# Optimization experiments

Measured on AMD Instinct MI355X. Metric: run time of the kernel, lower is better.

Reference implementation:

```python
import jax, jax.numpy as jnp
import numpy as np
import math

B, S, H, NH, NKV, HD = 1, 2048, 4096, 32, 8, 128
ROPE_THETA = 10000.0


def setup_inputs() -> dict:
    key = jax.random.key(0)
    ks = jax.random.split(key, 16)
    hidden_states = jax.random.normal(ks[0], (B, S, H), jnp.float32) * 0.02
    Wq = jax.random.normal(ks[1], (NH * HD, H), jnp.float32) * 0.02
    Wk = jax.random.normal(ks[2], (NKV * HD, H), jnp.float32) * 0.02
    Wv = jax.random.normal(ks[3], (NKV * HD, H), jnp.float32) * 0.02
    Wo = jax.random.normal(ks[4], (H, NH * HD), jnp.float32) * 0.02
    # RoPE cos/sin, HF Llama convention: emb = concat(freqs, freqs)
    inv_freq = 1.0 / (ROPE_THETA ** (jnp.arange(0, HD, 2, dtype=jnp.float32) / HD))
    pos = jnp.arange(S, dtype=jnp.float32)
    freqs = pos[:, None] * inv_freq[None, :]              # [S, HD/2]
    emb = jnp.concatenate([freqs, freqs], axis=-1)        # [S, HD]
    cos = jnp.cos(emb)[None]                              # [1, S, HD]
    sin = jnp.sin(emb)[None]
    # additive causal mask [B, 1, S, S]
    causal = jnp.tril(jnp.ones((S, S), dtype=bool))
    attention_mask = jnp.where(causal, 0.0, -1e9).astype(jnp.float32)[None, None]
    # reorder permutations (as written by GPTQ act-order reordering)
    perm = lambda k, n: jax.random.permutation(k, n).astype(jnp.int32)
    return {
        'hidden_states': hidden_states, 'Wq': Wq, 'Wk': Wk, 'Wv': Wv, 'Wo': Wo,
        'cos': cos, 'sin': sin, 'attention_mask': attention_mask,
        'q_order_col': perm(ks[5], H), 'q_order_row': perm(ks[6], NH * HD),
        'k_order_col': perm(ks[7], H), 'k_order_row': perm(ks[8], NKV * HD),
        'v_order_col': perm(ks[9], H), 'v_order_row': perm(ks[10], NKV * HD),
        'o_order_col': perm(ks[11], NH * HD), 'o_order_row': perm(ks[12], H),
    }


def _rotate_half(x):
    x1, x2 = jnp.split(x, 2, axis=-1)
    return jnp.concatenate([-x2, x1], axis=-1)


def reference(hidden_states, Wq, Wk, Wv, Wo, cos, sin, attention_mask,
              q_order_col, q_order_row, k_order_col, k_order_row,
              v_order_col, v_order_row, o_order_col, o_order_row):
    bsz, q_len, _ = hidden_states.shape
    # permuted projections: gather cols of input, GEMM, gather rows of output
    q = hidden_states[:, :, q_order_col] @ Wq.T
    q = q[:, :, q_order_row]
    k = hidden_states[:, :, k_order_col] @ Wk.T
    k = k[:, :, k_order_row]
    v = hidden_states[:, :, v_order_col] @ Wv.T
    v = v[:, :, v_order_row]
    q = q.reshape(bsz, q_len, NH, HD).transpose(0, 2, 1, 3)   # [B,NH,S,HD]
    k = k.reshape(bsz, q_len, NKV, HD).transpose(0, 2, 1, 3)  # [B,NKV,S,HD]
    v = v.reshape(bsz, q_len, NKV, HD).transpose(0, 2, 1, 3)
    # RoPE
    c = cos[:, None, :, :]  # [1,1,S,HD]
    s = sin[:, None, :, :]
    q = q * c + _rotate_half(q) * s
    k = k * c + _rotate_half(k) * s
    # repeat_kv for GQA
    rep = NH // NKV
    k = jnp.repeat(k, rep, axis=1)  # [B,NH,S,HD]
    v = jnp.repeat(v, rep, axis=1)
    # eager attention: full score matrix, fp32 softmax
    scores = jnp.einsum('bhqd,bhkd->bhqk', q, k) / math.sqrt(HD)
    scores = scores + attention_mask
    probs = jax.nn.softmax(scores.astype(jnp.float32), axis=-1).astype(q.dtype)
    # dropout p=0.0 (eval) -> identity
    attn = jnp.einsum('bhqk,bhkd->bhqd', probs, v)
    attn = attn.transpose(0, 2, 1, 3).reshape(bsz, q_len, NH * HD)
    out = attn[:, :, o_order_col] @ Wo.T
    out = out[:, :, o_order_row]
    return out
```

## Files before the change

kernel.cpp:

```cpp
#include <hip/hip_runtime.h>

typedef unsigned short u16;
typedef unsigned char u8;
typedef __bf16 bf16x8 __attribute__((ext_vector_type(8)));
typedef float f32x4 __attribute__((ext_vector_type(4)));
typedef int i32x4 __attribute__((ext_vector_type(4)));
typedef int i32x8 __attribute__((ext_vector_type(8)));

__device__ __forceinline__ u16 f2bf(float f) {
    unsigned u = __float_as_uint(f);
    unsigned r = (u + 0x7fffu + ((u >> 16) & 1u)) >> 16;
    return (u16)r;
}
__device__ __forceinline__ float bf2f(u16 h) {
    return __uint_as_float(((unsigned)h) << 16);
}
__device__ __forceinline__ unsigned pack_bf2(float lo, float hi) {
    unsigned a = __float_as_uint(hi) + 0x8000u;
    unsigned b = __float_as_uint(lo) + 0x8000u;
    return __builtin_amdgcn_perm(a, b, 0x07060302u);
}
__device__ __forceinline__ unsigned pack_fp8x4(float a, float b, float c, float d) {
    unsigned w = __builtin_amdgcn_cvt_pk_fp8_f32(a, b, 0, false);
    w = __builtin_amdgcn_cvt_pk_fp8_f32(c, d, w, true);
    return w;
}
__device__ __forceinline__ void async_copy16(const void* g, void* l) {
    __builtin_amdgcn_global_load_lds((__attribute__((address_space(1))) void*)(void*)g,
                                     (__attribute__((address_space(3))) void*)l, 16, 0, 0);
}

#define FP8_SCALE 64.0f
#define FP8_UNSCALE (1.0f / 4096.0f)


__global__ void inv4_k(const int* __restrict__ q, const int* __restrict__ k,
                       const int* __restrict__ v, const int* __restrict__ o,
                       int* __restrict__ invq, int* __restrict__ invk,
                       int* __restrict__ invv, int* __restrict__ invo) {
    int i = blockIdx.x * 256 + threadIdx.x;
    int a = i >> 12, j = i & 4095;
    const int* p = a == 0 ? q : a == 1 ? k : a == 2 ? v : o;
    int* inv = a == 0 ? invq : a == 1 ? invk : a == 2 ? invv : invo;
    inv[p[j]] = j;
}

__global__ __launch_bounds__(256) void permw4_k(
    const float* __restrict__ Wq, const float* __restrict__ Wk,
    const float* __restrict__ Wv, const float* __restrict__ Wo,
    const int* __restrict__ qor, const int* __restrict__ kor,
    const int* __restrict__ vor, const int* __restrict__ oor,
    const int* __restrict__ invq, const int* __restrict__ invk,
    const int* __restrict__ invv, const int* __restrict__ invo,
    u8* __restrict__ Wqkf8, u16* __restrict__ Wvp, u16* __restrict__ Wop) {
    __shared__ float rowbuf[4096];
    int j = blockIdx.x;
    const float* W; const int* rp; const int* inv; int row; int f8;
    u8* out8 = nullptr; u16* out16 = nullptr;
    if (j < 4096)      { W = Wq; rp = qor; inv = invq; row = j;        out8 = Wqkf8 + (size_t)j * 4096; f8 = 1; }
    else if (j < 5120) { W = Wk; rp = kor; inv = invk; row = j - 4096; out8 = Wqkf8 + (size_t)j * 4096; f8 = 1; }
    else if (j < 6144) { W = Wv; rp = vor; inv = invv; row = j - 5120; out16 = Wvp + (size_t)(j - 5120) * 4096; f8 = 0; }
    else               { W = Wo; rp = oor; inv = invo; row = j - 6144; out16 = Wop + (size_t)(j - 6144) * 4096; f8 = 0; }
    if (f8) {
        int hd = row & 127, b = hd >> 4;
        row = (row & ~127) | ((hd & 15) | ((b & 1) << 6) | ((b & 2) << 3) | ((hd & 64) >> 1));
    }
    const float4* wr4 = (const float4*)(W + (size_t)rp[row] * 4096);
#pragma unroll
    for (int t = 0; t < 4; t++)
        ((float4*)rowbuf)[threadIdx.x + t * 256] = wr4[threadIdx.x + t * 256];
    __syncthreads();
    if (f8) {
        int t = threadIdx.x;
        const int4* inv4p = (const int4*)inv;
        float v[16];
#pragma unroll
        for (int u = 0; u < 4; u++) {
            int4 ix = inv4p[t * 4 + u];
            v[4 * u + 0] = rowbuf[ix.x] * FP8_SCALE;
            v[4 * u + 1] = rowbuf[ix.y] * FP8_SCALE;
            v[4 * u + 2] = rowbuf[ix.z] * FP8_SCALE;
            v[4 * u + 3] = rowbuf[ix.w] * FP8_SCALE;
        }
        uint4 wv;
        wv.x = pack_fp8x4(v[0], v[1], v[2], v[3]);
        wv.y = pack_fp8x4(v[4], v[5], v[6], v[7]);
        wv.z = pack_fp8x4(v[8], v[9], v[10], v[11]);
        wv.w = pack_fp8x4(v[12], v[13], v[14], v[15]);
        int tb = (t & ~7) | ((t & 7) ^ (j & 7));
        ((uint4*)out8)[tb] = wv;
    } else {
        unsigned* o32 = (unsigned*)out16;
        const int2* inv2 = (const int2*)inv;
#pragma unroll
        for (int t = 0; t < 8; t++) {
            int c = threadIdx.x + t * 256;
            int2 ij = inv2[c];
            o32[c] = pack_bf2(rowbuf[ij.x], rowbuf[ij.y]);
        }
    }
}

__global__ __launch_bounds__(256) void cvt_k(const float* __restrict__ x,
                                             u16* __restrict__ Xb,
                                             u8* __restrict__ Xf8) {
    int row = blockIdx.x;
    int t = threadIdx.x;
    const float4* src = (const float4*)(x + (size_t)row * 4096);
    float v[16];
#pragma unroll
    for (int u = 0; u < 4; u++) {
        float4 a = src[t * 4 + u];
        v[4 * u + 0] = a.x; v[4 * u + 1] = a.y; v[4 * u + 2] = a.z; v[4 * u + 3] = a.w;
    }
    uint4 b0, b1;
    b0.x = pack_bf2(v[0], v[1]);  b0.y = pack_bf2(v[2], v[3]);
    b0.z = pack_bf2(v[4], v[5]);  b0.w = pack_bf2(v[6], v[7]);
    b1.x = pack_bf2(v[8], v[9]);  b1.y = pack_bf2(v[10], v[11]);
    b1.z = pack_bf2(v[12], v[13]); b1.w = pack_bf2(v[14], v[15]);
    uint4* ob = (uint4*)(Xb + (size_t)row * 4096);
    ob[t * 2] = b0;
    ob[t * 2 + 1] = b1;
    uint4 w8;
    w8.x = pack_fp8x4(v[0] * FP8_SCALE, v[1] * FP8_SCALE, v[2] * FP8_SCALE, v[3] * FP8_SCALE);
    w8.y = pack_fp8x4(v[4] * FP8_SCALE, v[5] * FP8_SCALE, v[6] * FP8_SCALE, v[7] * FP8_SCALE);
    w8.z = pack_fp8x4(v[8] * FP8_SCALE, v[9] * FP8_SCALE, v[10] * FP8_SCALE, v[11] * FP8_SCALE);
    w8.w = pack_fp8x4(v[12] * FP8_SCALE, v[13] * FP8_SCALE, v[14] * FP8_SCALE, v[15] * FP8_SCALE);
    int tb = (t & ~7) | ((t & 7) ^ (row & 7));
    ((uint4*)(Xf8 + (size_t)row * 4096))[tb] = w8;
}

__global__ __launch_bounds__(256) void vtr_k(const float* __restrict__ Vpart,
                                             u16* __restrict__ Vt) {
    __shared__ u16 t[64][65];
    int bx = blockIdx.x;
    int s0 = (bx & 31) * 64, c0 = (bx >> 5) * 64;
    int x = threadIdx.x & 63, y4 = threadIdx.x >> 6;
    const float* Vp0 = Vpart;
    const float* Vp1 = Vpart + (size_t)2048 * 1024;
    for (int i = 0; i < 16; i++) {
        int r = y4 * 16 + i;
        size_t idx = (size_t)(s0 + r) * 1024 + c0 + x;
        t[r][x] = f2bf(Vp0[idx] + Vp1[idx]);
    }
    __syncthreads();
    for (int i = 0; i < 16; i++) {
        int r = y4 * 16 + i;
        int xk = 4 * (x & 15) + (x >> 4);
        Vt[(size_t)(c0 + r) * 2048 + s0 + xk] = t[x][r];
    }
}


#define QKV_BAR() asm volatile("s_barrier" ::: "memory")

#define QK_STAGE(bufi, kt) do {                                                   \
    u8* la_ = S8 + (bufi) * 32768 + w * 4096;                                     \
    u8* lb_ = la_ + 16384;                                                        \
    const int k0_ = (kt) * 128;                                                   \
    _Pragma("unroll")                                                             \
    for (int t_ = 0; t_ < 4; t_++)                                                \
        async_copy16(AgQ + (size_t)t_ * 8 * 4096 + k0_, la_ + t_ * 1024);         \
    _Pragma("unroll")                                                             \
    for (int t_ = 0; t_ < 4; t_++)                                                \
        async_copy16(BgQ + (size_t)t_ * 8 * 4096 + k0_, lb_ + t_ * 1024);         \
} while (0)

#define QK_COMPUTE(bufi) do {                                                     \
    const u8* la_ = S8 + (bufi) * 32768;                                          \
    const u8* lb_ = la_ + 16384;                                                  \
    union { i32x8 v8; i32x4 v4[2]; } u_;                                          \
    i32x8 bfv[4], af0, af1;                                                       \
    _Pragma("unroll")                                                             \
    for (int j_ = 0; j_ < 4; j_++) {                                              \
        const int r_ = (wn + j_ * 16 + l16) * 128;                                \
        u_.v4[0] = *(const i32x4*)&lb_[r_ + s0b];                                 \
        u_.v4[1] = *(const i32x4*)&lb_[r_ + s1b];                                 \
        bfv[j_] = u_.v8;                                                          \
    }                                                                             \
    { const int r_ = (wm + l16) * 128;                                            \
      u_.v4[0] = *(const i32x4*)&la_[r_ + s0b];                                   \
      u_.v4[1] = *(const i32x4*)&la_[r_ + s1b]; af0 = u_.v8; }                    \
    { const int r_ = (wm + 16 + l16) * 128;                                       \
      u_.v4[0] = *(const i32x4*)&la_[r_ + s0b];                                   \
      u_.v4[1] = *(const i32x4*)&la_[r_ + s1b]; af1 = u_.v8; }                    \
    asm volatile("s_waitcnt lgkmcnt(0)" ::: "memory");                            \
    __builtin_amdgcn_sched_barrier(0);                                            \
    __builtin_amdgcn_s_setprio(1);                                                \
    _Pragma("unroll")                                                             \
    for (int j_ = 0; j_ < 4; j_++) {                                              \
        acc[0][j_] = __builtin_amdgcn_mfma_scale_f32_16x16x128_f8f6f4(af0, bfv[j_], acc[0][j_], 0, 0, 0, 0x7F7F7F7F, 0, 0x7F7F7F7F); \
        acc[1][j_] = __builtin_amdgcn_mfma_scale_f32_16x16x128_f8f6f4(af1, bfv[j_], acc[1][j_], 0, 0, 0, 0x7F7F7F7F, 0, 0x7F7F7F7F); \
    }                                                                             \
    __builtin_amdgcn_s_setprio(0);                                                \
    { const int r_ = (wm + 32 + l16) * 128;                                       \
      u_.v4[0] = *(const i32x4*)&la_[r_ + s0b];                                   \
      u_.v4[1] = *(const i32x4*)&la_[r_ + s1b]; af0 = u_.v8; }                    \
    { const int r_ = (wm + 48 + l16) * 128;                                       \
      u_.v4[0] = *(const i32x4*)&la_[r_ + s0b];                                   \
      u_.v4[1] = *(const i32x4*)&la_[r_ + s1b]; af1 = u_.v8; }                    \
    asm volatile("s_waitcnt lgkmcnt(0)" ::: "memory");                            \
    __builtin_amdgcn_sched_barrier(0);                                            \
    __builtin_amdgcn_s_setprio(1);                                                \
    _Pragma("unroll")                                                             \
    for (int j_ = 0; j_ < 4; j_++) {                                              \
        acc[2][j_] = __builtin_amdgcn_mfma_scale_f32_16x16x128_f8f6f4(af0, bfv[j_], acc[2][j_], 0, 0, 0, 0x7F7F7F7F, 0, 0x7F7F7F7F); \
        acc[3][j_] = __builtin_amdgcn_mfma_scale_f32_16x16x128_f8f6f4(af1, bfv[j_], acc[3][j_], 0, 0, 0, 0x7F7F7F7F, 0, 0x7F7F7F7F); \
    }                                                                             \
    __builtin_amdgcn_s_setprio(0);                                                \
} while (0)

#define V_STAGE(bufi, kt) do {                                                    \
    u16* a0_ = (u16*)(S8 + (bufi) * 32768);                                       \
    u16* a1_ = a0_ + 4096;                                                        \
    u16* b0_ = a0_ + 8192;                                                        \
    u16* b1_ = a0_ + 12288;                                                       \
    const int k0_ = (kt) * 64;                                                    \
    async_copy16(AgV + k0_,                          a0_ + w * 512);              \
    async_copy16(AgV + (size_t)64 * 4096 + k0_,      a0_ + (w + 4) * 512);        \
    async_copy16(AgV + k0_ + 32,                     a1_ + w * 512);              \
    async_copy16(AgV + (size_t)64 * 4096 + k0_ + 32, a1_ + (w + 4) * 512);        \
    async_copy16(BgV + k0_,                          b0_ + w * 512);              \
    async_copy16(BgV + (size_t)64 * 4096 + k0_,      b0_ + (w + 4) * 512);        \
    async_copy16(BgV + k0_ + 32,                     b1_ + w * 512);              \
    async_copy16(BgV + (size_t)64 * 4096 + k0_ + 32, b1_ + (w + 4) * 512);        \
} while (0)

#define V_COMPUTE(bufi) do {                                                      \
    const u16* base_ = (const u16*)(S8 + (bufi) * 32768);                         \
    _Pragma("unroll")                                                             \
    for (int kk_ = 0; kk_ < 2; kk_++) {                                           \
        const u16* la_ = base_ + kk_ * 4096;                                      \
        const u16* lb_ = base_ + 8192 + kk_ * 4096;                               \
        bf16x8 af[4], bfv[4];                                                     \
        _Pragma("unroll")                                                         \
        for (int i_ = 0; i_ < 4; i_++)                                            \
            af[i_] = *(const bf16x8*)&la_[(wm + i_ * 16 + l16) * 32 + quad * 8];  \
        _Pragma("unroll")                                                         \
        for (int j_ = 0; j_ < 4; j_++)                                            \
            bfv[j_] = *(const bf16x8*)&lb_[(wn + j_ * 16 + l16) * 32 + quad * 8]; \
        asm volatile("s_waitcnt lgkmcnt(0)" ::: "memory");                        \
        __builtin_amdgcn_sched_barrier(0);                                        \
        __builtin_amdgcn_s_setprio(1);                                            \
        _Pragma("unroll")                                                         \
        for (int i_ = 0; i_ < 4; i_++)                                            \
            _Pragma("unroll")                                                     \
            for (int j_ = 0; j_ < 4; j_++)                                        \
                acc[i_][j_] = __builtin_amdgcn_mfma_f32_16x16x32_bf16(af[i_], bfv[j_], acc[i_][j_], 0, 0, 0); \
        __builtin_amdgcn_s_setprio(0);                                            \
    }                                                                             \
} while (0)

__global__ __launch_bounds__(256, 2) void gemm_qkv_k(const u8* __restrict__ Xf8,
                                                     const u16* __restrict__ Xb,
                                                     const u8* __restrict__ Wqk,
                                                     const u16* __restrict__ Wv,
                                                     u16* __restrict__ QKV,
                                                     float* __restrict__ Vpart,
                                                     const float* __restrict__ cosv,
                                                     const float* __restrict__ sinv) {
    extern __shared__ u8 S8[];
    const int tid = threadIdx.x;
    const int w = tid >> 6, lane = tid & 63;
    const int quad = lane >> 4, l16 = lane & 15;
    const int bm0 = blockIdx.y * 128;
    const int wm = (w >> 1) * 64, wn = (w & 1) * 64;
    const int swz = l16 & 7;
    const int s0b = ((quad * 2) ^ swz) * 16;
    const int s1b = ((quad * 2 + 1) ^ swz) * 16;

    if (blockIdx.x < 40) {
        const int bn0 = blockIdx.x * 128;
        const u8* AgQ = Xf8 + (size_t)(bm0 + w * 32 + (lane >> 3)) * 4096 + (lane & 7) * 16;
        const u8* BgQ = Wqk + (size_t)(bn0 + w * 32 + (lane >> 3)) * 4096 + (lane & 7) * 16;
        f32x4 acc[4][4] = {};

        QK_STAGE(0, 0);
        QK_STAGE(1, 1);
        asm volatile("s_waitcnt vmcnt(8)" ::: "memory");
        QKV_BAR();
        int cur = 0;
        for (int t = 0; t < 30; ++t) {
            QK_COMPUTE(cur);
            QKV_BAR();
            QK_STAGE(cur, t + 2);
            asm volatile("s_waitcnt vmcnt(8)" ::: "memory");
            QKV_BAR();
            cur ^= 1;
        }
        QK_COMPUTE(0);
        asm volatile("s_waitcnt vmcnt(0)" ::: "memory");
        QKV_BAR();
        QK_COMPUTE(1);

        const float qsc = (bn0 < 4096) ? 0.1275174f : 1.0f;
        const int hb = (wn ? 32 : 0) + l16;
#pragma unroll
        for (int i = 0; i < 4; i++) {
            const int row = bm0 + wm + i * 16 + quad * 4;
#pragma unroll
            for (int jp = 0; jp < 2; jp++) {
                const int d1 = hb + jp * 16;
                const int ce = bn0 + wn + jp * 32 + l16;
#pragma unroll
                for (int r = 0; r < 4; r++) {
                    const int s = row + r;
                    const float c  = cosv[s * 128 + d1];
                    const float sn = sinv[s * 128 + d1];
                    const float x1 = acc[i][jp * 2][r]     * FP8_UNSCALE;
                    const float x2 = acc[i][jp * 2 + 1][r] * FP8_UNSCALE;
                    QKV[(size_t)s * 6144 + ce]      = f2bf((x1 * c - x2 * sn) * qsc);
                    QKV[(size_t)s * 6144 + ce + 16] = f2bf((x2 * c + x1 * sn) * qsc);
                }
            }
        }
    } else {
        const int vx = blockIdx.x - 40;
        const int bn0 = (vx & 7) * 128;
        const int kslice = vx >> 3;
        const int kb = kslice * 2048;
        const int r0 = w * 16 + (lane >> 2);
        const int c0 = (lane & 3) * 8;
        const u16* AgV = Xb + (size_t)(bm0 + r0) * 4096 + kb + c0;
        const u16* BgV = Wv + (size_t)(bn0 + r0) * 4096 + kb + c0;
        f32x4 acc[4][4] = {};

        V_STAGE(0, 0);
        V_STAGE(1, 1);
        asm volatile("s_waitcnt vmcnt(8)" ::: "memory");
        QKV_BAR();
        int cur = 0;
        for (int t = 0; t < 30; ++t) {
            V_COMPUTE(cur);
            QKV_BAR();
            V_STAGE(cur, t + 2);
            asm volatile("s_waitcnt vmcnt(8)" ::: "memory");
            QKV_BAR();
            cur ^= 1;
        }
        V_COMPUTE(0);
        asm volatile("s_waitcnt vmcnt(0)" ::: "memory");
        QKV_BAR();
        V_COMPUTE(1);

        float* Vp = Vpart + (size_t)kslice * 2048 * 1024;
#pragma unroll
        for (int i = 0; i < 4; i++) {
            const int row = bm0 + wm + i * 16 + quad * 4;
#pragma unroll
            for (int j = 0; j < 4; j++) {
                const int col = bn0 + wn + j * 16 + l16;
#pragma unroll
                for (int r = 0; r < 4; r++)
                    Vp[(size_t)(row + r) * 1024 + col] = acc[i][j][r];
            }
        }
    }
}


#define GO_STAGE(bufi, kt) do {                                                   \
    u16* la_ = S + (bufi) * 24576;                                                \
    u16* lb_ = la_ + 16384;                                                       \
    const int k0_ = (kt) * 64;                                                    \
    _Pragma("unroll")                                                             \
    for (int u = 0; u < 4; u++)                                                   \
        async_copy16(Asrc + (size_t)u * 64 * 4096 + k0_, la_ + u * 4096 + sdst);  \
    _Pragma("unroll")                                                             \
    for (int u = 0; u < 2; u++)                                                   \
        async_copy16(Bsrc + (size_t)u * 64 * 4096 + k0_, lb_ + u * 4096 + sdst);  \
} while (0)

#define GO_COMPUTE(bufi) do {                                                     \
    const u16* la_ = S + (bufi) * 24576;                                          \
    const u16* lb_ = la_ + 16384;                                                 \
    bf16x8 bfr[4][2], afr[2][2];                                                  \
    _Pragma("unroll")                                                             \
    for (int j = 0; j < 4; j++) {                                                 \
        const int rb_ = (wn + j * 16 + l16) * 64;                                 \
        bfr[j][0] = *(const bf16x8*)&lb_[rb_ + o0];                               \
        bfr[j][1] = *(const bf16x8*)&lb_[rb_ + o1];                               \
    }                                                                             \
    _Pragma("unroll")                                                             \
    for (int i = 0; i < 2; i++) {                                                 \
        const int ra_ = (wm + i * 16 + l16) * 64;                                 \
        afr[i][0] = *(const bf16x8*)&la_[ra_ + o0];                               \
        afr[i][1] = *(const bf16x8*)&la_[ra_ + o1];                               \
    }                                                                             \
    asm volatile("s_waitcnt lgkmcnt(0)" ::: "memory");                            \
    __builtin_amdgcn_sched_barrier(0);                                            \
    __builtin_amdgcn_s_setprio(1);                                                \
    _Pragma("unroll")                                                             \
    for (int i = 0; i < 2; i++)                                                   \
        _Pragma("unroll")                                                         \
        for (int j = 0; j < 4; j++) {                                             \
            acc[i][j] = __builtin_amdgcn_mfma_f32_16x16x32_bf16(afr[i][0], bfr[j][0], acc[i][j], 0, 0, 0); \
            acc[i][j] = __builtin_amdgcn_mfma_f32_16x16x32_bf16(afr[i][1], bfr[j][1], acc[i][j], 0, 0, 0); \
        }                                                                         \
    __builtin_amdgcn_s_setprio(0);                                                \
    _Pragma("unroll")                                                             \
    for (int i = 0; i < 2; i++) {                                                 \
        const int ra_ = (wm + (i + 2) * 16 + l16) * 64;                           \
        afr[i][0] = *(const bf16x8*)&la_[ra_ + o0];                               \
        afr[i][1] = *(const bf16x8*)&la_[ra_ + o1];                               \
    }                                                                             \
    asm volatile("s_waitcnt lgkmcnt(0)" ::: "memory");                            \
    __builtin_amdgcn_sched_barrier(0);                                            \
    __builtin_amdgcn_s_setprio(1);                                                \
    _Pragma("unroll")                                                             \
    for (int i = 0; i < 2; i++)                                                   \
        _Pragma("unroll")                                                         \
        for (int j = 0; j < 4; j++) {                                             \
            acc[i + 2][j] = __builtin_amdgcn_mfma_f32_16x16x32_bf16(afr[i][0], bfr[j][0], acc[i + 2][j], 0, 0, 0); \
            acc[i + 2][j] = __builtin_amdgcn_mfma_f32_16x16x32_bf16(afr[i][1], bfr[j][1], acc[i + 2][j], 0, 0, 0); \
        }                                                                         \
    __builtin_amdgcn_s_setprio(0);                                                \
} while (0)

#define GO_BAR() asm volatile("s_barrier" ::: "memory")

__global__ __launch_bounds__(512, 2) void gemm_o_k(const u16* __restrict__ A,
                                                   const u16* __restrict__ B,
                                                   float* __restrict__ Out) {
    extern __shared__ u16 S[];
    const int tid = threadIdx.x;
    const int w = tid >> 6, lane = tid & 63;
    const int quad = lane >> 4, l16 = lane & 15;
    const int linear = blockIdx.y * 32 + blockIdx.x;
    const int wgid = (linear & 7) * 32 + (linear >> 3);
    const int bm0 = (wgid >> 5) * 256;
    const int bn0 = (wgid & 31) * 128;
    const int wm = (w >> 1) * 64;
    const int wn = (w & 1) * 64;
    const int sr = tid >> 3;
    const int scg = ((tid & 7) ^ (sr & 7)) * 8;
    const int sdst = tid * 8;
    const u16* Asrc = A + (size_t)(bm0 + sr) * 4096 + scg;
    const u16* Bsrc = B + (size_t)(bn0 + sr) * 4096 + scg;
    const int swz = l16 & 7;
    const int o0 = (quad ^ swz) * 8;
    const int o1 = ((4 | quad) ^ swz) * 8;

    f32x4 acc[4][4] = {};

    GO_STAGE(0, 0);
    GO_STAGE(1, 1);
    GO_STAGE(2, 2);
    asm volatile("s_waitcnt vmcnt(12)" ::: "memory");
    GO_BAR();

    int cur = 0;
    for (int t = 0; t < 61; ++t) {
        GO_COMPUTE(cur);
        GO_BAR();
        GO_STAGE(cur, t + 3);
        asm volatile("s_waitcnt vmcnt(12)" ::: "memory");
        GO_BAR();
        cur = (cur == 2) ? 0 : cur + 1;
    }
    GO_COMPUTE(1);
    asm volatile("s_waitcnt vmcnt(6)" ::: "memory");
    GO_BAR();
    GO_COMPUTE(2);
    asm volatile("s_waitcnt vmcnt(0)" ::: "memory");
    GO_BAR();
    GO_COMPUTE(0);

#pragma unroll
    for (int i = 0; i < 4; i++) {
        const int row = bm0 + wm + i * 16 + quad * 4;
#pragma unroll
        for (int j = 0; j < 4; j++) {
            const int col = bn0 + wn + j * 16 + l16;
#pragma unroll
            for (int r = 0; r < 4; r++)
                Out[(size_t)(row + r) * 4096 + col] = acc[i][j][r];
        }
    }
}


__global__ __launch_bounds__(512) void attn_k(const u16* __restrict__ Qb,
                                              const u16* __restrict__ Kb,
                                              const u16* __restrict__ Vt,
                                              u16* __restrict__ Ob,
                                              int qstride, int kstride) {
    __shared__ u16 ldsK[4 * 64 * 32];
    __shared__ u16 ldsV[2 * 128 * 32];
    __shared__ u16 ldsP[8][16 * 72];
    const int h = blockIdx.x;
    const int kvh = h >> 2;
    const int tid = threadIdx.x;
    const int w = tid >> 6, lane = tid & 63;
    const int quad = lane >> 4, l16 = lane & 15;

    const u16* kp0[2]; const u16* vp0[2];
    u16* ldk[2]; u16* ldv[2];
#pragma unroll
    for (int t = 0; t < 2; t++) {
        int wl = w + t * 8;
        int kk = wl >> 2, part = wl & 3;
        kp0[t] = Kb + (size_t)(part * 16 + (lane >> 2)) * kstride + kvh * 128 + kk * 32 + (lane & 3) * 8;
        int ks2 = wl >> 3, p2 = wl & 7;
        vp0[t] = Vt + (size_t)(kvh * 128 + p2 * 16 + (lane >> 2)) * 2048 + ks2 * 32 + (lane & 3) * 8;
        ldk[t] = ldsK + wl * 512;
        ldv[t] = ldsV + wl * 512;
    }

#pragma unroll
    for (int ph = 0; ph < 2; ph++) {
        const int qt = ph == 0 ? (15 - (int)blockIdx.y) : (int)blockIdx.y;
        const int q0 = qt * 128;
        const int wrow = q0 + w * 16;

        bf16x8 qf[4];
#pragma unroll
        for (int kk = 0; kk < 4; kk++)
            qf[kk] = *(const bf16x8*)&Qb[(size_t)(wrow + l16) * qstride +
                                         h * 128 + kk * 32 + quad * 8];

        const u16* kp[2]; const u16* vp[2];
        kp[0] = kp0[0]; kp[1] = kp0[1];
        vp[0] = vp0[0]; vp[1] = vp0[1];

        f32x4 acc_o[8] = {};
        float lrow[4] = {};

        const int nk = 2 * (qt + 1);
        for (int kn = 0; kn < nk; kn++) {
            const int g0 = kn * 64;
            async_copy16(kp[0], ldk[0]);
            async_copy16(kp[1], ldk[1]);
            async_copy16(vp[0], ldv[0]);
            async_copy16(vp[1], ldv[1]);
            kp[0] += (size_t)64 * kstride; kp[1] += (size_t)64 * kstride;
            vp[0] += 64; vp[1] += 64;
            __syncthreads();

            if (g0 <= wrow + 15) {
                f32x4 accs[4] = {};
#pragma unroll
                for (int kk = 0; kk < 4; kk++) {
                    bf16x8 bfrag[4];
#pragma unroll
                    for (int ni = 0; ni < 4; ni++)
                        bfrag[ni] = *(const bf16x8*)&ldsK[kk * 2048 + (ni * 16 + l16) * 32 + quad * 8];
                    __builtin_amdgcn_s_setprio(1);
#pragma unroll
                    for (int ni = 0; ni < 4; ni++)
                        accs[ni] = __builtin_amdgcn_mfma_f32_16x16x32_bf16(
                            qf[kk], bfrag[ni], accs[ni], 0, 0, 0);
                    __builtin_amdgcn_s_setprio(0);
                }
                const bool diag = (g0 + 63 > wrow);
                int kidx[4];
#pragma unroll
                for (int ni = 0; ni < 4; ni++) kidx[ni] = g0 + ni * 16 + l16;
#pragma unroll
                for (int r = 0; r < 4; r++) {
                    const int qrow = wrow + quad * 4 + r;
                    float p[4];
#pragma unroll
                    for (int ni = 0; ni < 4; ni++) {
                        float s = accs[ni][r];
                        if (diag && (kidx[ni] > qrow)) s = -1e30f;
                        p[ni] = __builtin_amdgcn_exp2f(s);
                    }
                    lrow[r] += (p[0] + p[1]) + (p[2] + p[3]);
                    uint2 pk;
                    pk.x = pack_bf2(p[0], p[1]);
                    pk.y = pack_bf2(p[2], p[3]);
                    *(uint2*)&ldsP[w][(quad * 4 + r) * 72 + l16 * 4] = pk;
                }
#pragma unroll
                for (int ks = 0; ks < 2; ks++) {
                    bf16x8 pa = *(const bf16x8*)&ldsP[w][l16 * 72 + ks * 32 + quad * 8];
                    __builtin_amdgcn_s_setprio(1);
#pragma unroll
                    for (int oj = 0; oj < 8; oj++) {
                        bf16x8 vb = *(const bf16x8*)&ldsV[ks * 4096 + (oj * 16 + l16) * 32 + quad * 8];
                        acc_o[oj] = __builtin_amdgcn_mfma_f32_16x16x32_bf16(
                            pa, vb, acc_o[oj], 0, 0, 0);
                    }
                    __builtin_amdgcn_s_setprio(0);
                }
            }
            __syncthreads();
        }

#pragma unroll
        for (int r = 0; r < 4; r++) {
            float l = lrow[r];
            l += __shfl_xor(l, 1);
            l += __shfl_xor(l, 2);
            l += __shfl_xor(l, 4);
            l += __shfl_xor(l, 8);
            const float inv = 1.0f / l;
            const int qrow = wrow + quad * 4 + r;
#pragma unroll
            for (int oj = 0; oj < 8; oj++)
                Ob[(size_t)qrow * 4096 + h * 128 + oj * 16 + l16] =
                    f2bf(acc_o[oj][r] * inv);
        }
    }
}


extern "C" void kernel_launch(void* const* d_in, const int* in_sizes, int n_in,
                              void* d_out, int out_size, void* d_ws, size_t ws_size,
                              hipStream_t stream) {
    (void)in_sizes; (void)n_in; (void)out_size; (void)ws_size;
    const float* hidden = (const float*)d_in[0];
    const float* Wq = (const float*)d_in[1];
    const float* Wk = (const float*)d_in[2];
    const float* Wv = (const float*)d_in[3];
    const float* Wo = (const float*)d_in[4];
    const float* cosv = (const float*)d_in[5];
    const float* sinv = (const float*)d_in[6];
    const int* qoc = (const int*)d_in[8];
    const int* qor = (const int*)d_in[9];
    const int* koc = (const int*)d_in[10];
    const int* kor = (const int*)d_in[11];
    const int* voc = (const int*)d_in[12];
    const int* vor = (const int*)d_in[13];
    const int* ooc = (const int*)d_in[14];
    const int* oor = (const int*)d_in[15];

    char* ws = (char*)d_ws;
    size_t off = 0;
    int* invq = (int*)(ws + off); off += 16384;
    int* invk = (int*)(ws + off); off += 16384;
    int* invv = (int*)(ws + off); off += 16384;
    int* invo = (int*)(ws + off); off += 16384;
    u16* Wop   = (u16*)(ws + off); off += (size_t)4096 * 4096 * 2;
    u16* Xb    = (u16*)(ws + off); off += (size_t)2048 * 4096 * 2;
    u8*  Wqkf8 = (u8*)(ws + off);  off += (size_t)5120 * 4096;
    u16* Wvp   = (u16*)(ws + off); off += (size_t)1024 * 4096 * 2;
    u8*  Xf8   = (u8*)(ws + off);  off += (size_t)2048 * 4096;
    u16* QKVb  = (u16*)(ws + off); off += (size_t)2048 * 6144 * 2;
    u16* Vtb   = (u16*)(ws + off); off += (size_t)1024 * 2048 * 2;
    float* Vpart = (float*)(ws + off); off += (size_t)2 * 2048 * 1024 * 4;
    u16* Attb  = Xb;

    inv4_k<<<64, 256, 0, stream>>>(qoc, koc, voc, ooc, invq, invk, invv, invo);
    permw4_k<<<10240, 256, 0, stream>>>(Wq, Wk, Wv, Wo, qor, kor, vor, oor,
                                        invq, invk, invv, invo, Wqkf8, Wvp, Wop);
    cvt_k<<<2048, 256, 0, stream>>>(hidden, Xb, Xf8);

    gemm_qkv_k<<<dim3(56, 16), 256, 65536, stream>>>(Xf8, Xb, Wqkf8, Wvp, QKVb, Vpart,
                                                     cosv, sinv);

    vtr_k<<<512, 256, 0, stream>>>(Vpart, Vtb);

    attn_k<<<dim3(32, 8), 512, 0, stream>>>(QKVb, QKVb + 4096, Vtb, Attb, 6144, 6144);

    gemm_o_k<<<dim3(32, 8), 512, 147456, stream>>>(Attb, Wop, (float*)d_out);
}
```

Before: 468.0 us.

## Double-buffer K/V tiles in attention kernel and swizzle LDS layout

Splits the attention kernel's K and V shared-memory tiles into two buffers, so the async copy of tile kn+2 is issued while tile kn is being computed, with vmcnt waits and barriers in place of the single-buffer load-then-sync pattern. It also XOR-swizzles the 16-byte column block in both the global-to-LDS copy and the fragment reads to reduce LDS bank conflicts. The cost is twice the LDS footprint for K and V, which may lower occupancy, plus an extra barrier at the end of each phase.

```diff
diff --git a/kernel.cpp b/kernel.cpp
--- a/kernel.cpp
+++ b/kernel.cpp
@@ -480,31 +480,95 @@
 }
 
 
+#define ATT_STAGE(bufi, g) do {                                                   \
+    const size_t go_ = (size_t)(g) * 64;                                          \
+    async_copy16(kbase0 + go_ * kstride, ldk0[bufi]);                             \
+    async_copy16(kbase1 + go_ * kstride, ldk1[bufi]);                             \
+    async_copy16(vbase0 + go_, ldv0[bufi]);                                       \
+    async_copy16(vbase1 + go_, ldv1[bufi]);                                       \
+} while (0)
+
+#define ATT_COMPUTE(bufi, g0) do {                                                \
+    if ((g0) <= wrow + 15) {                                                      \
+        const u16* lK_ = ldsK[bufi];                                              \
+        const u16* lV_ = ldsV[bufi];                                              \
+        f32x4 accs[4] = {};                                                       \
+        _Pragma("unroll")                                                         \
+        for (int kk = 0; kk < 4; kk++) {                                          \
+            bf16x8 bfrag[4];                                                      \
+            _Pragma("unroll")                                                     \
+            for (int ni = 0; ni < 4; ni++)                                        \
+                bfrag[ni] = *(const bf16x8*)&lK_[kk * 2048 + (ni * 16 + l16) * 32 + sswz]; \
+            __builtin_amdgcn_s_setprio(1);                                        \
+            _Pragma("unroll")                                                     \
+            for (int ni = 0; ni < 4; ni++)                                        \
+                accs[ni] = __builtin_amdgcn_mfma_f32_16x16x32_bf16(               \
+                    qf[kk], bfrag[ni], accs[ni], 0, 0, 0);                        \
+            __builtin_amdgcn_s_setprio(0);                                        \
+        }                                                                         \
+        const bool diag = ((g0) + 63 > wrow);                                     \
+        int kidx[4];                                                              \
+        _Pragma("unroll")                                                         \
+        for (int ni = 0; ni < 4; ni++) kidx[ni] = (g0) + ni * 16 + l16;           \
+        _Pragma("unroll")                                                         \
+        for (int r = 0; r < 4; r++) {                                             \
+            const int qrow = wrow + quad * 4 + r;                                 \
+            float p[4];                                                           \
+            _Pragma("unroll")                                                     \
+            for (int ni = 0; ni < 4; ni++) {                                      \
+                float s = accs[ni][r];                                            \
+                if (diag && (kidx[ni] > qrow)) s = -1e30f;                        \
+                p[ni] = __builtin_amdgcn_exp2f(s);                                \
+            }                                                                     \
+            lrow[r] += (p[0] + p[1]) + (p[2] + p[3]);                             \
+            uint2 pk;                                                             \
+            pk.x = pack_bf2(p[0], p[1]);                                          \
+            pk.y = pack_bf2(p[2], p[3]);                                          \
+            *(uint2*)&ldsP[w][(quad * 4 + r) * 72 + l16 * 4] = pk;                \
+        }                                                                         \
+        _Pragma("unroll")                                                         \
+        for (int ks = 0; ks < 2; ks++) {                                          \
+            bf16x8 pa = *(const bf16x8*)&ldsP[w][l16 * 72 + ks * 32 + quad * 8];  \
+            __builtin_amdgcn_s_setprio(1);                                        \
+            _Pragma("unroll")                                                     \
+            for (int oj = 0; oj < 8; oj++) {                                      \
+                bf16x8 vb = *(const bf16x8*)&lV_[ks * 4096 + (oj * 16 + l16) * 32 + sswz]; \
+                acc_o[oj] = __builtin_amdgcn_mfma_f32_16x16x32_bf16(              \
+                    pa, vb, acc_o[oj], 0, 0, 0);                                  \
+            }                                                                     \
+            __builtin_amdgcn_s_setprio(0);                                        \
+        }                                                                         \
+    }                                                                             \
+} while (0)
+
 __global__ __launch_bounds__(512) void attn_k(const u16* __restrict__ Qb,
                                               const u16* __restrict__ Kb,
                                               const u16* __restrict__ Vt,
                                               u16* __restrict__ Ob,
                                               int qstride, int kstride) {
-    __shared__ u16 ldsK[4 * 64 * 32];
-    __shared__ u16 ldsV[2 * 128 * 32];
+    __shared__ u16 ldsK[2][4 * 64 * 32];
+    __shared__ u16 ldsV[2][2 * 128 * 32];
     __shared__ u16 ldsP[8][16 * 72];
     const int h = blockIdx.x;
     const int kvh = h >> 2;
     const int tid = threadIdx.x;
     const int w = tid >> 6, lane = tid & 63;
     const int quad = lane >> 4, l16 = lane & 15;
-
-    const u16* kp0[2]; const u16* vp0[2];
-    u16* ldk[2]; u16* ldv[2];
-#pragma unroll
-    for (int t = 0; t < 2; t++) {
-        int wl = w + t * 8;
-        int kk = wl >> 2, part = wl & 3;
-        kp0[t] = Kb + (size_t)(part * 16 + (lane >> 2)) * kstride + kvh * 128 + kk * 32 + (lane & 3) * 8;
-        int ks2 = wl >> 3, p2 = wl & 7;
-        vp0[t] = Vt + (size_t)(kvh * 128 + p2 * 16 + (lane >> 2)) * 2048 + ks2 * 32 + (lane & 3) * 8;
-        ldk[t] = ldsK + wl * 512;
-        ldv[t] = ldsV + wl * 512;
+    const int sswz = (quad ^ ((l16 >> 1) & 3)) * 8;
+
+    const int cblk = (lane & 3) ^ ((lane >> 3) & 3);
+    const int wlA = w, wlB = w + 8;
+    const u16* kbase0 = Kb + (size_t)((wlA & 3) * 16 + (lane >> 2)) * kstride + kvh * 128 + (wlA >> 2) * 32 + cblk * 8;
+    const u16* kbase1 = Kb + (size_t)((wlB & 3) * 16 + (lane >> 2)) * kstride + kvh * 128 + (wlB >> 2) * 32 + cblk * 8;
+    const u16* vbase0 = Vt + (size_t)(kvh * 128 + (wlA & 7) * 16 + (lane >> 2)) * 2048 + (wlA >> 3) * 32 + cblk * 8;
+    const u16* vbase1 = Vt + (size_t)(kvh * 128 + (wlB & 7) * 16 + (lane >> 2)) * 2048 + (wlB >> 3) * 32 + cblk * 8;
+    u16* ldk0[2]; u16* ldk1[2]; u16* ldv0[2]; u16* ldv1[2];
+#pragma unroll
+    for (int b = 0; b < 2; b++) {
+        ldk0[b] = &ldsK[b][wlA * 512];
+        ldk1[b] = &ldsK[b][wlB * 512];
+        ldv0[b] = &ldsV[b][wlA * 512];
+        ldv1[b] = &ldsV[b][wlB * 512];
     }
 
 #pragma unroll
@@ -519,74 +583,27 @@
             qf[kk] = *(const bf16x8*)&Qb[(size_t)(wrow + l16) * qstride +
                                          h * 128 + kk * 32 + quad * 8];
 
-        const u16* kp[2]; const u16* vp[2];
-        kp[0] = kp0[0]; kp[1] = kp0[1];
-        vp[0] = vp0[0]; vp[1] = vp0[1];
-
         f32x4 acc_o[8] = {};
         float lrow[4] = {};
 
         const int nk = 2 * (qt + 1);
-        for (int kn = 0; kn < nk; kn++) {
-            const int g0 = kn * 64;
-            async_copy16(kp[0], ldk[0]);
-            async_copy16(kp[1], ldk[1]);
-            async_copy16(vp[0], ldv[0]);
-            async_copy16(vp[1], ldv[1]);
-            kp[0] += (size_t)64 * kstride; kp[1] += (size_t)64 * kstride;
-            vp[0] += 64; vp[1] += 64;
-            __syncthreads();
-
-            if (g0 <= wrow + 15) {
-                f32x4 accs[4] = {};
-#pragma unroll
-                for (int kk = 0; kk < 4; kk++) {
-                    bf16x8 bfrag[4];
-#pragma unroll
-                    for (int ni = 0; ni < 4; ni++)
-                        bfrag[ni] = *(const bf16x8*)&ldsK[kk * 2048 + (ni * 16 + l16) * 32 + quad * 8];
-                    __builtin_amdgcn_s_setprio(1);
-#pragma unroll
-                    for (int ni = 0; ni < 4; ni++)
-                        accs[ni] = __builtin_amdgcn_mfma_f32_16x16x32_bf16(
-                            qf[kk], bfrag[ni], accs[ni], 0, 0, 0);
-                    __builtin_amdgcn_s_setprio(0);
-                }
-                const bool diag = (g0 + 63 > wrow);
-                int kidx[4];
-#pragma unroll
-                for (int ni = 0; ni < 4; ni++) kidx[ni] = g0 + ni * 16 + l16;
-#pragma unroll
-                for (int r = 0; r < 4; r++) {
-                    const int qrow = wrow + quad * 4 + r;
-                    float p[4];
-#pragma unroll
-                    for (int ni = 0; ni < 4; ni++) {
-                        float s = accs[ni][r];
-                        if (diag && (kidx[ni] > qrow)) s = -1e30f;
-                        p[ni] = __builtin_amdgcn_exp2f(s);
-                    }
-                    lrow[r] += (p[0] + p[1]) + (p[2] + p[3]);
-                    uint2 pk;
-                    pk.x = pack_bf2(p[0], p[1]);
-                    pk.y = pack_bf2(p[2], p[3]);
-                    *(uint2*)&ldsP[w][(quad * 4 + r) * 72 + l16 * 4] = pk;
-                }
-#pragma unroll
-                for (int ks = 0; ks < 2; ks++) {
-                    bf16x8 pa = *(const bf16x8*)&ldsP[w][l16 * 72 + ks * 32 + quad * 8];
-                    __builtin_amdgcn_s_setprio(1);
-#pragma unroll
-                    for (int oj = 0; oj < 8; oj++) {
-                        bf16x8 vb = *(const bf16x8*)&ldsV[ks * 4096 + (oj * 16 + l16) * 32 + quad * 8];
-                        acc_o[oj] = __builtin_amdgcn_mfma_f32_16x16x32_bf16(
-                            pa, vb, acc_o[oj], 0, 0, 0);
-                    }
-                    __builtin_amdgcn_s_setprio(0);
-                }
-            }
-            __syncthreads();
-        }
+        ATT_STAGE(0, 0);
+        ATT_STAGE(1, 1);
+        asm volatile("s_waitcnt vmcnt(4)" ::: "memory");
+        QKV_BAR();
+        int cur = 0;
+        for (int kn = 0; kn < nk - 2; kn++) {
+            ATT_COMPUTE(cur, kn * 64);
+            QKV_BAR();
+            ATT_STAGE(cur, kn + 2);
+            asm volatile("s_waitcnt vmcnt(4)" ::: "memory");
+            QKV_BAR();
+            cur ^= 1;
+        }
+        ATT_COMPUTE(cur, (nk - 2) * 64);
+        asm volatile("s_waitcnt vmcnt(0)" ::: "memory");
+        QKV_BAR();
+        ATT_COMPUTE(cur ^ 1, (nk - 1) * 64);
 
 #pragma unroll
         for (int r = 0; r < 4; r++) {
@@ -602,6 +619,7 @@
                 Ob[(size_t)qrow * 4096 + h * 128 + oj * 16 + l16] =
                     f2bf(acc_o[oj][r] * inv);
         }
+        QKV_BAR();
     }
 }
 
```

After: 451.0 us. 1.04x faster.
